# Optimization experiments

Measured on AMD Instinct MI355X. Metric: run time of the kernel, lower is better.

The kernel has to match this reference:

```python
import jax, jax.numpy as jnp
import numpy as np

N_NODES = 100000
IN_C, HID_C, OUT_C = 128, 64, 16
N_EDGES = 3200000


def gcn_conv(x, W, b, src, dst, deg_inv_sqrt, n_nodes):
    """PyG GCNConv: out = D^-1/2 (A+I) D^-1/2 (x @ W) + b.
    src/dst already include self-loops; deg_inv_sqrt precomputed."""
    h = x @ W  # [N, out_c]
    norm = deg_inv_sqrt[src] * deg_inv_sqrt[dst]  # [E+N]
    msg = h[src] * norm[:, None]                  # gather + scale
    out = jax.ops.segment_sum(msg, dst, num_segments=n_nodes)
    return out + b


def _prep_edges(edge_index, n_nodes):
    loops = jnp.arange(n_nodes, dtype=edge_index.dtype)
    src = jnp.concatenate([edge_index[0], loops])
    dst = jnp.concatenate([edge_index[1], loops])
    deg = jax.ops.segment_sum(jnp.ones_like(dst, dtype=jnp.float32), dst,
                              num_segments=n_nodes)
    deg_inv_sqrt = jnp.where(deg > 0, jax.lax.rsqrt(jnp.maximum(deg, 1.0)), 0.0)
    return src, dst, deg_inv_sqrt


def setup_inputs() -> dict:
    key = jax.random.key(0)
    ks = jax.random.split(key, 8)
    x = jax.random.normal(ks[0], (N_NODES, IN_C), dtype=jnp.float32)
    edge_index = jax.random.randint(ks[1], (2, N_EDGES), 0, N_NODES, dtype=jnp.int64)
    # Glorot-ish init for GCN weights
    W1 = jax.random.normal(ks[2], (IN_C, HID_C), dtype=jnp.float32) / np.sqrt(IN_C)
    b1 = jnp.zeros((HID_C,), dtype=jnp.float32)
    W_mu = jax.random.normal(ks[3], (HID_C, OUT_C), dtype=jnp.float32) / np.sqrt(HID_C)
    b_mu = jnp.zeros((OUT_C,), dtype=jnp.float32)
    W_ls = jax.random.normal(ks[4], (HID_C, OUT_C), dtype=jnp.float32) / np.sqrt(HID_C)
    b_ls = jnp.zeros((OUT_C,), dtype=jnp.float32)
    return {"x": x, "edge_index": edge_index, "W1": W1, "b1": b1,
            "W_mu": W_mu, "b_mu": b_mu, "W_ls": W_ls, "b_ls": b_ls}


def reference(x, edge_index, W1, b1, W_mu, b_mu, W_ls, b_ls):
    n = x.shape[0]
    src, dst, dis = _prep_edges(edge_index, n)
    # conv1 -> relu (dropout is identity in eval mode)
    h = jax.nn.relu(gcn_conv(x, W1, b1, src, dst, dis, n))
    mu = gcn_conv(h, W_mu, b_mu, src, dst, dis, n)
    logstd = gcn_conv(h, W_ls, b_ls, src, dst, dis, n)
    return (mu, logstd)
```

## Files before the change

### kernel.cpp

```cpp
#include <hip/hip_runtime.h>
#include <hip/hip_bf16.h>

#define HIDC 64
#define INC 128
#define OUTC 16
#define NBLK 512
#define BSHIFT 8
#define MAXBUCK 512

typedef __attribute__((ext_vector_type(8))) short bf16x8;
typedef __attribute__((ext_vector_type(4))) float f32x4;

__device__ __forceinline__ float bflo(unsigned int u) {
    return __uint_as_float(u << 16);
}
__device__ __forceinline__ float bfhi(unsigned int u) {
    return __uint_as_float(u & 0xffff0000u);
}
__device__ __forceinline__ unsigned int f2bf(float f) {
    unsigned int b = __float_as_uint(f);
    return (b + 0x7fffu + ((b >> 16) & 1u)) >> 16;
}

__global__ __launch_bounds__(256) void count_pass(const int* __restrict__ dst,
                                                  int* __restrict__ bcnt,
                                                  int n_edges, int nbuck) {
    __shared__ int lh[MAXBUCK];
    for (int i = threadIdx.x; i < nbuck; i += 256) lh[i] = 0;
    __syncthreads();
    const int chunk = (n_edges + NBLK - 1) / NBLK;
    const int begin = blockIdx.x * chunk;
    const int end = min(begin + chunk, n_edges);
    for (int e = begin + threadIdx.x; e < end; e += 256) {
        int d = __builtin_nontemporal_load(dst + e);
        atomicAdd(&lh[d >> BSHIFT], 1);
    }
    __syncthreads();
    for (int i = threadIdx.x; i < nbuck; i += 256)
        bcnt[blockIdx.x * nbuck + i] = lh[i];
}

__device__ __forceinline__ int xphys(int j, int nbuck) {
    return (j & (NBLK - 1)) * nbuck + (j >> 9);
}

__global__ __launch_bounds__(256) void mscan_k1(const int* __restrict__ bcnt,
                                                int* __restrict__ partial,
                                                int m, int nbuck) {
    int base = blockIdx.x * 1024;
    int lim = min(base + 1024, m);
    int s = 0;
    for (int j = base + threadIdx.x; j < lim; j += 256) s += bcnt[xphys(j, nbuck)];
    #pragma unroll
    for (int d = 32; d; d >>= 1) s += __shfl_down(s, d);
    __shared__ int wsum[4];
    if ((threadIdx.x & 63) == 0) wsum[threadIdx.x >> 6] = s;
    __syncthreads();
    if (threadIdx.x == 0) partial[blockIdx.x] = wsum[0] + wsum[1] + wsum[2] + wsum[3];
}

__global__ __launch_bounds__(256) void mscan_k2(const int* __restrict__ partial,
                                                int* __restrict__ pbase, int nblk) {
    __shared__ int sh[256];
    int v = (threadIdx.x < nblk) ? partial[threadIdx.x] : 0;
    sh[threadIdx.x] = v;
    __syncthreads();
    for (int d = 1; d < 256; d <<= 1) {
        int t = (threadIdx.x >= d) ? sh[threadIdx.x - d] : 0;
        __syncthreads();
        sh[threadIdx.x] += t;
        __syncthreads();
    }
    if (threadIdx.x < nblk) pbase[threadIdx.x] = sh[threadIdx.x] - v;
}

__global__ __launch_bounds__(256) void mscan_k3(const int* __restrict__ bcnt,
                                                const int* __restrict__ pbase,
                                                int* __restrict__ bofs,
                                                int m, int nbuck) {
    int j0 = blockIdx.x * 1024 + threadIdx.x * 4;
    int c0 = (j0 + 0 < m) ? bcnt[xphys(j0 + 0, nbuck)] : 0;
    int c1 = (j0 + 1 < m) ? bcnt[xphys(j0 + 1, nbuck)] : 0;
    int c2 = (j0 + 2 < m) ? bcnt[xphys(j0 + 2, nbuck)] : 0;
    int c3 = (j0 + 3 < m) ? bcnt[xphys(j0 + 3, nbuck)] : 0;
    int tsum = c0 + c1 + c2 + c3;
    __shared__ int sh[256];
    sh[threadIdx.x] = tsum;
    __syncthreads();
    for (int d = 1; d < 256; d <<= 1) {
        int t = (threadIdx.x >= d) ? sh[threadIdx.x - d] : 0;
        __syncthreads();
        sh[threadIdx.x] += t;
        __syncthreads();
    }
    int pre = pbase[blockIdx.x] + sh[threadIdx.x] - tsum;
    if (j0 + 0 < m) bofs[xphys(j0 + 0, nbuck)] = pre;
    if (j0 + 1 < m) bofs[xphys(j0 + 1, nbuck)] = pre + c0;
    if (j0 + 2 < m) bofs[xphys(j0 + 2, nbuck)] = pre + c0 + c1;
    if (j0 + 3 < m) bofs[xphys(j0 + 3, nbuck)] = pre + c0 + c1 + c2;
}

__global__ __launch_bounds__(256) void place_pass(const int* __restrict__ src,
                                                  const int* __restrict__ dst,
                                                  const int* __restrict__ bofs,
                                                  int* __restrict__ pairs,
                                                  int n_edges, int nbuck) {
    __shared__ int lcur[MAXBUCK];
    for (int i = threadIdx.x; i < nbuck; i += 256)
        lcur[i] = bofs[blockIdx.x * nbuck + i];
    __syncthreads();
    const int chunk = (n_edges + NBLK - 1) / NBLK;
    const int begin = blockIdx.x * chunk;
    const int end = min(begin + chunk, n_edges);
    for (int e = begin + threadIdx.x; e < end; e += 256) {
        int d = __builtin_nontemporal_load(dst + e);
        int s = __builtin_nontemporal_load(src + e);
        int slot = atomicAdd(&lcur[d >> BSHIFT], 1);
        pairs[slot] = s | ((d & 255) << 17);
    }
}

__global__ __launch_bounds__(256) void csr_bucket(const int* __restrict__ pairs,
                                                  const int* __restrict__ bofs,
                                                  int* __restrict__ off,
                                                  float* __restrict__ dis,
                                                  int* __restrict__ csr,
                                                  int n_nodes, int n_edges, int nbuck) {
    __shared__ int hist[256];
    __shared__ int lofs[256];
    __shared__ int ss[256];
    const int b = blockIdx.x;
    const int node0 = b << BSHIFT;
    const int nn = min(256, n_nodes - node0);
    const int pbeg = bofs[b];
    const int pend = (b + 1 < nbuck) ? bofs[b + 1] : n_edges;
    const int tid = threadIdx.x;
    hist[tid] = 0;
    __syncthreads();
    for (int i = pbeg + tid; i < pend; i += 256)
        atomicAdd(&hist[pairs[i] >> 17], 1);
    __syncthreads();
    int h0 = (tid < nn) ? hist[tid] : 0;
    ss[tid] = h0;
    __syncthreads();
    for (int d = 1; d < 256; d <<= 1) {
        int t = (tid >= d) ? ss[tid - d] : 0;
        __syncthreads();
        ss[tid] += t;
        __syncthreads();
    }
    int pre = pbeg + ss[tid] - h0;
    if (tid < nn) {
        lofs[tid] = pre;
        off[node0 + tid] = pre;
        dis[node0 + tid] = rsqrtf((float)(h0 + 1));
    }
    __syncthreads();
    for (int i = pbeg + tid; i < pend; i += 256) {
        int v = pairs[i];
        int slot = atomicAdd(&lofs[v >> 17], 1);
        csr[slot] = v & 0x1FFFF;
    }
    if (b == 0 && tid == 0) off[n_nodes] = n_edges;
}

__global__ __launch_bounds__(256) void gemm1_mfma(const float* __restrict__ x,
                                                  const float* __restrict__ W,
                                                  unsigned int* __restrict__ xWb,
                                                  int n_nodes) {
    __shared__ unsigned short WbT[64][136];
    __shared__ unsigned short xs[64][136];
    const int tid = threadIdx.x;
    const int lane = tid & 63, wave = tid >> 6;
    const int quad = lane >> 4, l16 = lane & 15;
    for (int i = tid; i < INC * HIDC; i += 256) {
        int k = i >> 6, n = i & 63;
        WbT[n][k] = (unsigned short)f2bf(W[i]);
    }
    __syncthreads();
    bf16x8 bfr[4][4];
    #pragma unroll
    for (int nt = 0; nt < 4; ++nt)
        #pragma unroll
        for (int kt = 0; kt < 4; ++kt)
            bfr[nt][kt] = *(const bf16x8*)&WbT[nt * 16 + l16][kt * 32 + quad * 8];

    for (int base = blockIdx.x * 64; base < n_nodes; base += gridDim.x * 64) {
        int nrows = min(64, n_nodes - base);
        __syncthreads();
        for (int i = tid; i < nrows * 32; i += 256) {
            int m = i >> 5, kq = i & 31;
            float4 v = ((const float4*)(x + (size_t)(base + m) * INC))[kq];
            unsigned int* xp = (unsigned int*)&xs[m][kq * 4];
            xp[0] = f2bf(v.x) | (f2bf(v.y) << 16);
            xp[1] = f2bf(v.z) | (f2bf(v.w) << 16);
        }
        __syncthreads();
        int mrow = wave * 16;
        if (mrow < nrows) {
            bf16x8 af[4];
            #pragma unroll
            for (int kt = 0; kt < 4; ++kt)
                af[kt] = *(const bf16x8*)&xs[mrow + l16][kt * 32 + quad * 8];
            f32x4 acc[4];
            #pragma unroll
            for (int nt = 0; nt < 4; ++nt) acc[nt] = (f32x4){0.f, 0.f, 0.f, 0.f};
            #pragma unroll
            for (int kt = 0; kt < 4; ++kt)
                #pragma unroll
                for (int nt = 0; nt < 4; ++nt)
                    acc[nt] = __builtin_amdgcn_mfma_f32_16x16x32_bf16(
                        af[kt], bfr[nt][kt], acc[nt], 0, 0, 0);
            #pragma unroll
            for (int nt = 0; nt < 4; ++nt) {
                #pragma unroll
                for (int r = 0; r < 4; ++r) {
                    unsigned int bv = f2bf(acc[nt][r]);
                    unsigned int hv = (unsigned int)__shfl_down((int)bv, 1);
                    int row = base + mrow + quad * 4 + r;
                    if (!(l16 & 1) && row < n_nodes)
                        xWb[((size_t)row * 64 + nt * 16 + l16) >> 1] = bv | (hv << 16);
                }
            }
        }
    }
}

__global__ __launch_bounds__(256) void gemm2_mfma(const uint4* __restrict__ hb4,
                                                  const float* __restrict__ Wmu,
                                                  const float* __restrict__ Wls,
                                                  unsigned int* __restrict__ hwb,
                                                  int n_nodes) {
    __shared__ unsigned short WT2[32][72];
    __shared__ unsigned short hs[64][72];
    const int tid = threadIdx.x;
    const int lane = tid & 63, wave = tid >> 6;
    const int quad = lane >> 4, l16 = lane & 15;
    for (int i = tid; i < HIDC * 32; i += 256) {
        int n = i & 31, k = i >> 5;
        float v = (n < 16) ? Wmu[k * 16 + n] : Wls[k * 16 + (n - 16)];
        WT2[n][k] = (unsigned short)f2bf(v);
    }
    __syncthreads();
    bf16x8 bfr[2][2];
    #pragma unroll
    for (int nt = 0; nt < 2; ++nt)
        #pragma unroll
        for (int kt = 0; kt < 2; ++kt)
            bfr[nt][kt] = *(const bf16x8*)&WT2[nt * 16 + l16][kt * 32 + quad * 8];

    for (int base = blockIdx.x * 64; base < n_nodes; base += gridDim.x * 64) {
        int nrows = min(64, n_nodes - base);
        __syncthreads();
        for (int i = tid; i < nrows * 8; i += 256) {
            int m = i >> 3, q = i & 7;
            uint4 v = hb4[(size_t)(base + m) * 8 + q];
            unsigned int* hp = (unsigned int*)&hs[m][q * 8];
            hp[0] = v.x; hp[1] = v.y; hp[2] = v.z; hp[3] = v.w;
        }
        __syncthreads();
        int mrow = wave * 16;
        if (mrow < nrows) {
            bf16x8 af[2];
            #pragma unroll
            for (int kt = 0; kt < 2; ++kt)
                af[kt] = *(const bf16x8*)&hs[mrow + l16][kt * 32 + quad * 8];
            f32x4 acc[2];
            #pragma unroll
            for (int nt = 0; nt < 2; ++nt) acc[nt] = (f32x4){0.f, 0.f, 0.f, 0.f};
            #pragma unroll
            for (int kt = 0; kt < 2; ++kt)
                #pragma unroll
                for (int nt = 0; nt < 2; ++nt)
                    acc[nt] = __builtin_amdgcn_mfma_f32_16x16x32_bf16(
                        af[kt], bfr[nt][kt], acc[nt], 0, 0, 0);
            #pragma unroll
            for (int nt = 0; nt < 2; ++nt) {
                #pragma unroll
                for (int r = 0; r < 4; ++r) {
                    unsigned int bv = f2bf(acc[nt][r]);
                    unsigned int hv = (unsigned int)__shfl_down((int)bv, 1);
                    int row = base + mrow + quad * 4 + r;
                    if (!(l16 & 1) && row < n_nodes)
                        hwb[((size_t)row * 32 + nt * 16 + l16) >> 1] = bv | (hv << 16);
                }
            }
        }
    }
}

__global__ __launch_bounds__(256) void gather64(const uint2* __restrict__ xWb2,
                                                uint2* __restrict__ hb2,
                                                const int* __restrict__ csr,
                                                const int* __restrict__ off,
                                                const float* __restrict__ dis,
                                                const float* __restrict__ b1,
                                                int n_nodes) {
    const int tid = threadIdx.x;
    const int lane = tid & 63;
    const int grp = lane >> 4;
    const int l16 = lane & 15;
    int node = blockIdx.x * 16 + (tid >> 6) * 4 + grp;
    int beg = 0, end = 0;
    float dn = 0.f;
    if (node < n_nodes) {
        beg = off[node];
        end = off[node + 1];
        dn = dis[node];
    }
    float a0 = 0.f, a1 = 0.f, a2 = 0.f, a3 = 0.f;
    int e = beg;
    for (; e + 2 <= end; e += 2) {
        int s0 = csr[e], s1 = csr[e + 1];
        float n0 = dis[s0] * dn, n1 = dis[s1] * dn;
        uint2 r0 = xWb2[(size_t)s0 * 16 + l16];
        uint2 r1 = xWb2[(size_t)s1 * 16 + l16];
        a0 += bflo(r0.x) * n0; a1 += bfhi(r0.x) * n0;
        a2 += bflo(r0.y) * n0; a3 += bfhi(r0.y) * n0;
        a0 += bflo(r1.x) * n1; a1 += bfhi(r1.x) * n1;
        a2 += bflo(r1.y) * n1; a3 += bfhi(r1.y) * n1;
    }
    if (e < end) {
        int s0 = csr[e];
        float n0 = dis[s0] * dn;
        uint2 r0 = xWb2[(size_t)s0 * 16 + l16];
        a0 += bflo(r0.x) * n0; a1 += bfhi(r0.x) * n0;
        a2 += bflo(r0.y) * n0; a3 += bfhi(r0.y) * n0;
    }
    if (node < n_nodes) {
        uint2 r = xWb2[(size_t)node * 16 + l16];
        float s2 = dn * dn;
        a0 += bflo(r.x) * s2; a1 += bfhi(r.x) * s2;
        a2 += bflo(r.y) * s2; a3 += bfhi(r.y) * s2;
        float4 b = ((const float4*)b1)[l16];
        uint2 u;
        u.x = f2bf(fmaxf(a0 + b.x, 0.f)) | (f2bf(fmaxf(a1 + b.y, 0.f)) << 16);
        u.y = f2bf(fmaxf(a2 + b.z, 0.f)) | (f2bf(fmaxf(a3 + b.w, 0.f)) << 16);
        hb2[(size_t)node * 16 + l16] = u;
    }
}

__global__ __launch_bounds__(256) void gather32(const uint2* __restrict__ hwb2,
                                                const int* __restrict__ csr,
                                                const int* __restrict__ off,
                                                const float* __restrict__ dis,
                                                const float* __restrict__ bmu,
                                                const float* __restrict__ bls,
                                                float* __restrict__ out,
                                                int n_nodes) {
    const int tid = threadIdx.x;
    const int lane = tid & 63;
    const int grp = lane >> 3;
    const int l8 = lane & 7;
    int node = blockIdx.x * 32 + (tid >> 6) * 8 + grp;
    int beg = 0, end = 0;
    float dn = 0.f;
    if (node < n_nodes) {
        beg = off[node];
        end = off[node + 1];
        dn = dis[node];
    }
    float a0 = 0.f, a1 = 0.f, a2 = 0.f, a3 = 0.f;
    int e = beg;
    for (; e + 2 <= end; e += 2) {
        int s0 = csr[e], s1 = csr[e + 1];
        float n0 = dis[s0] * dn, n1 = dis[s1] * dn;
        uint2 r0 = hwb2[(size_t)s0 * 8 + l8];
        uint2 r1 = hwb2[(size_t)s1 * 8 + l8];
        a0 += bflo(r0.x) * n0; a1 += bfhi(r0.x) * n0;
        a2 += bflo(r0.y) * n0; a3 += bfhi(r0.y) * n0;
        a0 += bflo(r1.x) * n1; a1 += bfhi(r1.x) * n1;
        a2 += bflo(r1.y) * n1; a3 += bfhi(r1.y) * n1;
    }
    if (e < end) {
        int s0 = csr[e];
        float n0 = dis[s0] * dn;
        uint2 r0 = hwb2[(size_t)s0 * 8 + l8];
        a0 += bflo(r0.x) * n0; a1 += bfhi(r0.x) * n0;
        a2 += bflo(r0.y) * n0; a3 += bfhi(r0.y) * n0;
    }
    if (node < n_nodes) {
        uint2 r = hwb2[(size_t)node * 8 + l8];
        float s2 = dn * dn;
        a0 += bflo(r.x) * s2; a1 += bfhi(r.x) * s2;
        a2 += bflo(r.y) * s2; a3 += bfhi(r.y) * s2;
        float4 b = (l8 < 4) ? ((const float4*)bmu)[l8] : ((const float4*)bls)[l8 - 4];
        float4 o;
        o.x = a0 + b.x; o.y = a1 + b.y; o.z = a2 + b.z; o.w = a3 + b.w;
        if (l8 < 4)
            ((float4*)out)[(size_t)node * 4 + l8] = o;
        else
            ((float4*)out)[((size_t)n_nodes + node) * 4 + (l8 - 4)] = o;
    }
}

extern "C" void kernel_launch(void* const* d_in, const int* in_sizes, int n_in,
                              void* d_out, int out_size, void* d_ws, size_t ws_size,
                              hipStream_t stream) {
    const float* x   = (const float*)d_in[0];
    const int*   ei  = (const int*)d_in[1];
    const float* W1  = (const float*)d_in[2];
    const float* b1  = (const float*)d_in[3];
    const float* Wmu = (const float*)d_in[4];
    const float* bmu = (const float*)d_in[5];
    const float* Wls = (const float*)d_in[6];
    const float* bls = (const float*)d_in[7];
    float* out = (float*)d_out;

    const int N = in_sizes[0] / INC;
    const int E = in_sizes[1] / 2;
    const int* src = ei;
    const int* dst = ei + E;
    const int NBUCK = (N + 255) >> BSHIFT;
    const int M = NBUCK * NBLK;
    const int SBM = (M + 1023) / 1024;

    float* ws   = (float*)d_ws;
    float* dis  = ws;
    int*   off  = (int*)(ws + 131072);
    int*   bcnt = (int*)(ws + 262144);
    int*   bofs = (int*)(ws + 462336);
    int*   partial = (int*)(ws + 662528);
    int*   pbase   = partial + 256;
    int*   csr  = (int*)(ws + 663040);
    unsigned int* xWb = (unsigned int*)(ws + 663040 + (size_t)E);
    unsigned int* hb  = xWb + (size_t)N * 32;
    int*   pairs = (int*)hb;
    unsigned int* hwb = xWb;

    count_pass<<<NBLK, 256, 0, stream>>>(dst, bcnt, E, NBUCK);
    mscan_k1<<<SBM, 256, 0, stream>>>(bcnt, partial, M, NBUCK);
    mscan_k2<<<1, 256, 0, stream>>>(partial, pbase, SBM);
    mscan_k3<<<SBM, 256, 0, stream>>>(bcnt, pbase, bofs, M, NBUCK);
    place_pass<<<NBLK, 256, 0, stream>>>(src, dst, bofs, pairs, E, NBUCK);
    csr_bucket<<<NBUCK, 256, 0, stream>>>(pairs, bofs, off, dis, csr, N, E, NBUCK);

    gemm1_mfma<<<512, 256, 0, stream>>>(x, W1, xWb, N);
    gather64<<<(N + 15) / 16, 256, 0, stream>>>((const uint2*)xWb, (uint2*)hb,
                                                csr, off, dis, b1, N);

    gemm2_mfma<<<512, 256, 0, stream>>>((const uint4*)hb, Wmu, Wls, hwb, N);
    gather32<<<(N + 31) / 32, 256, 0, stream>>>((const uint2*)hwb, csr, off, dis,
                                                bmu, bls, out, N);
}
```

Baseline: 350.1 us.

## Pack quantized source norm into CSR entries and unroll gathers by four

Adds a pass that stores each edge's source deg^-1/2, quantized to 15 bits, in the upper bits of the CSR index word. Both gather kernels then read the normalization from the CSR word instead of doing a second random lookup into dis per edge. The gather loops are also unrolled from two to four edges to keep more loads in flight. In exchange there is an extra pass over the edge array, a small quantization error in the edge norms, and the assumption that node ids fit in 17 bits.

Result: faster. 338.3 us (-3.4%).

```diff
diff --git a/kernel.cpp b/kernel.cpp
--- a/kernel.cpp
+++ b/kernel.cpp
@@ -164,6 +164,17 @@
     if (b == 0 && tid == 0) off[n_nodes] = n_edges;
 }
 
+__global__ __launch_bounds__(256) void pack_norm(int* __restrict__ csr,
+                                                 const float* __restrict__ dis,
+                                                 int n_edges) {
+    int e = blockIdx.x * 256 + threadIdx.x;
+    if (e < n_edges) {
+        int s = csr[e];
+        int q = (int)(dis[s] * 32767.f + 0.5f);
+        csr[e] = s | (q << 17);
+    }
+}
+
 __global__ __launch_bounds__(256) void gemm1_mfma(const float* __restrict__ x,
                                                   const float* __restrict__ W,
                                                   unsigned int* __restrict__ xWb,
@@ -301,33 +312,42 @@
     const int grp = lane >> 4;
     const int l16 = lane & 15;
     int node = blockIdx.x * 16 + (tid >> 6) * 4 + grp;
-    int beg = 0, end = 0;
-    float dn = 0.f;
-    if (node < n_nodes) {
-        beg = off[node];
-        end = off[node + 1];
-        dn = dis[node];
-    }
+    if (node >= n_nodes) return;
+    const int beg = off[node], end = off[node + 1];
+    const float dn = dis[node];
+    const float dnq = dn * (1.0f / 32767.0f);
     float a0 = 0.f, a1 = 0.f, a2 = 0.f, a3 = 0.f;
     int e = beg;
-    for (; e + 2 <= end; e += 2) {
-        int s0 = csr[e], s1 = csr[e + 1];
-        float n0 = dis[s0] * dn, n1 = dis[s1] * dn;
-        uint2 r0 = xWb2[(size_t)s0 * 16 + l16];
-        uint2 r1 = xWb2[(size_t)s1 * 16 + l16];
+    for (; e + 4 <= end; e += 4) {
+        unsigned int v0 = (unsigned int)csr[e];
+        unsigned int v1 = (unsigned int)csr[e + 1];
+        unsigned int v2 = (unsigned int)csr[e + 2];
+        unsigned int v3 = (unsigned int)csr[e + 3];
+        uint2 r0 = xWb2[(size_t)(v0 & 0x1FFFF) * 16 + l16];
+        uint2 r1 = xWb2[(size_t)(v1 & 0x1FFFF) * 16 + l16];
+        uint2 r2 = xWb2[(size_t)(v2 & 0x1FFFF) * 16 + l16];
+        uint2 r3 = xWb2[(size_t)(v3 & 0x1FFFF) * 16 + l16];
+        float n0 = (float)(v0 >> 17) * dnq;
+        float n1 = (float)(v1 >> 17) * dnq;
+        float n2 = (float)(v2 >> 17) * dnq;
+        float n3 = (float)(v3 >> 17) * dnq;
         a0 += bflo(r0.x) * n0; a1 += bfhi(r0.x) * n0;
         a2 += bflo(r0.y) * n0; a3 += bfhi(r0.y) * n0;
         a0 += bflo(r1.x) * n1; a1 += bfhi(r1.x) * n1;
         a2 += bflo(r1.y) * n1; a3 += bfhi(r1.y) * n1;
-    }
-    if (e < end) {
-        int s0 = csr[e];
-        float n0 = dis[s0] * dn;
-        uint2 r0 = xWb2[(size_t)s0 * 16 + l16];
+        a0 += bflo(r2.x) * n2; a1 += bfhi(r2.x) * n2;
+        a2 += bflo(r2.y) * n2; a3 += bfhi(r2.y) * n2;
+        a0 += bflo(r3.x) * n3; a1 += bfhi(r3.x) * n3;
+        a2 += bflo(r3.y) * n3; a3 += bfhi(r3.y) * n3;
+    }
+    for (; e < end; ++e) {
+        unsigned int v0 = (unsigned int)csr[e];
+        uint2 r0 = xWb2[(size_t)(v0 & 0x1FFFF) * 16 + l16];
+        float n0 = (float)(v0 >> 17) * dnq;
         a0 += bflo(r0.x) * n0; a1 += bfhi(r0.x) * n0;
         a2 += bflo(r0.y) * n0; a3 += bfhi(r0.y) * n0;
     }
-    if (node < n_nodes) {
+    {
         uint2 r = xWb2[(size_t)node * 16 + l16];
         float s2 = dn * dn;
         a0 += bflo(r.x) * s2; a1 += bfhi(r.x) * s2;
@@ -353,33 +373,42 @@
     const int grp = lane >> 3;
     const int l8 = lane & 7;
     int node = blockIdx.x * 32 + (tid >> 6) * 8 + grp;
-    int beg = 0, end = 0;
-    float dn = 0.f;
-    if (node < n_nodes) {
-        beg = off[node];
-        end = off[node + 1];
-        dn = dis[node];
-    }
+    if (node >= n_nodes) return;
+    const int beg = off[node], end = off[node + 1];
+    const float dn = dis[node];
+    const float dnq = dn * (1.0f / 32767.0f);
     float a0 = 0.f, a1 = 0.f, a2 = 0.f, a3 = 0.f;
     int e = beg;
-    for (; e + 2 <= end; e += 2) {
-        int s0 = csr[e], s1 = csr[e + 1];
-        float n0 = dis[s0] * dn, n1 = dis[s1] * dn;
-        uint2 r0 = hwb2[(size_t)s0 * 8 + l8];
-        uint2 r1 = hwb2[(size_t)s1 * 8 + l8];
+    for (; e + 4 <= end; e += 4) {
+        unsigned int v0 = (unsigned int)csr[e];
+        unsigned int v1 = (unsigned int)csr[e + 1];
+        unsigned int v2 = (unsigned int)csr[e + 2];
+        unsigned int v3 = (unsigned int)csr[e + 3];
+        uint2 r0 = hwb2[(size_t)(v0 & 0x1FFFF) * 8 + l8];
+        uint2 r1 = hwb2[(size_t)(v1 & 0x1FFFF) * 8 + l8];
+        uint2 r2 = hwb2[(size_t)(v2 & 0x1FFFF) * 8 + l8];
+        uint2 r3 = hwb2[(size_t)(v3 & 0x1FFFF) * 8 + l8];
+        float n0 = (float)(v0 >> 17) * dnq;
+        float n1 = (float)(v1 >> 17) * dnq;
+        float n2 = (float)(v2 >> 17) * dnq;
+        float n3 = (float)(v3 >> 17) * dnq;
         a0 += bflo(r0.x) * n0; a1 += bfhi(r0.x) * n0;
         a2 += bflo(r0.y) * n0; a3 += bfhi(r0.y) * n0;
         a0 += bflo(r1.x) * n1; a1 += bfhi(r1.x) * n1;
         a2 += bflo(r1.y) * n1; a3 += bfhi(r1.y) * n1;
-    }
-    if (e < end) {
-        int s0 = csr[e];
-        float n0 = dis[s0] * dn;
-        uint2 r0 = hwb2[(size_t)s0 * 8 + l8];
+        a0 += bflo(r2.x) * n2; a1 += bfhi(r2.x) * n2;
+        a2 += bflo(r2.y) * n2; a3 += bfhi(r2.y) * n2;
+        a0 += bflo(r3.x) * n3; a1 += bfhi(r3.x) * n3;
+        a2 += bflo(r3.y) * n3; a3 += bfhi(r3.y) * n3;
+    }
+    for (; e < end; ++e) {
+        unsigned int v0 = (unsigned int)csr[e];
+        uint2 r0 = hwb2[(size_t)(v0 & 0x1FFFF) * 8 + l8];
+        float n0 = (float)(v0 >> 17) * dnq;
         a0 += bflo(r0.x) * n0; a1 += bfhi(r0.x) * n0;
         a2 += bflo(r0.y) * n0; a3 += bfhi(r0.y) * n0;
     }
-    if (node < n_nodes) {
+    {
         uint2 r = hwb2[(size_t)node * 8 + l8];
         float s2 = dn * dn;
         a0 += bflo(r.x) * s2; a1 += bfhi(r.x) * s2;
@@ -434,6 +463,7 @@
     mscan_k3<<<SBM, 256, 0, stream>>>(bcnt, pbase, bofs, M, NBUCK);
     place_pass<<<NBLK, 256, 0, stream>>>(src, dst, bofs, pairs, E, NBUCK);
     csr_bucket<<<NBUCK, 256, 0, stream>>>(pairs, bofs, off, dis, csr, N, E, NBUCK);
+    pack_norm<<<(E + 255) / 256, 256, 0, stream>>>(csr, dis, E);
 
     gemm1_mfma<<<512, 256, 0, stream>>>(x, W1, xWb, N);
     gather64<<<(N + 15) / 16, 256, 0, stream>>>((const uint2*)xWb, (uint2*)hb,
```
